# Optimization experiments

Hardware: AMD Instinct MI355X
Metric: run time of the kernel (lower is better)

The kernel has to match this reference:

```python
import jax, jax.numpy as jnp
import numpy as np

DELTA_A, DELTA_R = 0.1, 1.0
ALPHA, BETA, GAMMA = 1.0, 1.0, 0.001


def setup_inputs() -> dict:
    key = jax.random.key(0)
    B, D, H, W, K = 4, 32, 512, 512, 16
    out = jax.random.normal(key, (B, D, H, W), dtype=jnp.float32)
    # 4x4 block partition -> K=16 instance labels, one center per block
    gh, gw = 4, 4
    bh, bw = H // gh, W // gw
    rows = np.arange(H) // bh  # [H]
    cols = np.arange(W) // bw  # [W]
    labels = (rows[:, None] * gw + cols[None, :]).astype(np.int32)  # [H,W]
    target = jnp.asarray(np.broadcast_to(labels, (B, H, W)).copy())
    ctr = np.array([[r * bh + bh // 2, c * bw + bw // 2]
                    for r in range(gh) for c in range(gw)], dtype=np.int32)  # [K,2]
    centers = jnp.asarray(np.broadcast_to(ctr, (B, K, 2)).copy())
    return {"out": out, "target": target, "centers": centers, "batch_size": B}


def _safe_sqrt(x):
    # matches torch.linalg.norm subgradient 0 at 0 (avoids NaN grads)
    pos = x > 0
    return jnp.where(pos, jnp.sqrt(jnp.where(pos, x, 1.0)), 0.0)


def _pairwise_norm(a, b):
    # a [M,D], b [N,D] -> [M,N] euclidean distances via gram trick
    d2 = (jnp.sum(a * a, 1)[:, None] + jnp.sum(b * b, 1)[None, :]
          - 2.0 * a @ b.T)
    return _safe_sqrt(jax.nn.relu(d2))


def _per_image(o, t, c):
    # o [D,H,W], t [H,W] int, c [K,2] int
    D = o.shape[0]
    K = c.shape[0]
    x = o.reshape(D, -1).T                      # [HW, D]
    E = o[:, c[:, 0], c[:, 1]].T                # [K, D] center embeddings
    lab_c = t[c[:, 0], c[:, 1]]                 # [K]
    mask = (t.reshape(-1)[None, :] == lab_c[:, None])  # [K, HW]
    # attraction: hinged distance of every cluster pixel to its center
    norms = _pairwise_norm(E, x)                # [K, HW]
    hinged = jax.nn.relu(norms - DELTA_A) * mask
    cnt = jnp.sum(mask, axis=1)
    denom = jnp.maximum(cnt - 1, 1).astype(o.dtype)
    s_att = jnp.sum(jnp.sum(hinged, axis=1) / denom)
    # repelling: pairwise center distances; diagonal contributes relu(delta_r)
    # per row and the original subtracts delta_r per center -> excluded
    nE = _pairwise_norm(E, E)                   # [K, K]
    s_rep = jnp.sum(jax.nn.relu(DELTA_R - nE)) - K * DELTA_R
    # regularization: norm of each center embedding
    s_reg = jnp.sum(_safe_sqrt(jnp.sum(E * E, axis=1)))
    return s_att, s_rep, s_reg


def reference(out, target, centers, batch_size):
    K = centers.shape[1]
    s_att, s_rep, s_reg = jax.vmap(_per_image)(out, target, centers)  # [B] each
    div_att = jnp.float32(K)
    div_rep = jnp.float32(K * (K - 1))
    div_reg = jnp.float32(K)

    def step(carry, s):
        a, r, g = carry
        sa, sr, sg = s
        return ((a + sa) / div_att, (r + sr) / div_rep, (g + sg) / div_reg), None

    zero = jnp.float32(0.0)
    (att, rep, reg), _ = jax.lax.scan(step, (zero, zero, zero),
                                      (s_att, s_rep, s_reg))
    loss = ALPHA * att + BETA * rep + GAMMA * reg
    return loss, att, rep
```

## Files before the change

kernel.cpp:

```cpp
#include <hip/hip_runtime.h>
#include <hip/hip_bf16.h>

#define B_ 4
#define D_ 32
#define H_ 512
#define W_ 512
#define K_ 16
#define N_ (H_ * W_)
#define NQ_ (N_ / 4)
#define NBLK_ 256
#define EPAD 33

#define WS_SUM  0
#define WS_CNT  64
#define WS_E2   128
#define WS_LAB  192
#define WS_E    264
#define WS_PART 4096

typedef float vfloat4 __attribute__((ext_vector_type(4)));
typedef int vint4 __attribute__((ext_vector_type(4)));

__device__ inline vfloat4 nt_load_f4(const float* p) {
  return __builtin_nontemporal_load((const vfloat4*)p);
}
__device__ inline vint4 nt_load_i4(const int* p) {
  return __builtin_nontemporal_load((const vint4*)p);
}

__global__ __launch_bounds__(64) void setup_kernel(
    const float* __restrict__ outp, const int* __restrict__ target,
    const int* __restrict__ centers, float* __restrict__ ws) {
  const int b = blockIdx.x, k = blockIdx.y;
  const int lane = threadIdx.x;
  const int cy = centers[(b * K_ + k) * 2 + 0];
  const int cx = centers[(b * K_ + k) * 2 + 1];
  float v = 0.0f;
  if (lane < D_) {
    v = outp[(((size_t)b * D_ + lane) * H_ + cy) * W_ + cx];
    ws[WS_E + (b * K_ + k) * D_ + lane] = v;
  }
  float s = v * v;
  for (int off = 32; off > 0; off >>= 1) s += __shfl_xor(s, off, 64);
  if (lane == 0) {
    ws[WS_E2 + b * K_ + k] = s;
    ((int*)ws)[WS_LAB + b * K_ + k] = target[(size_t)b * N_ + cy * W_ + cx];
  }
}

__global__ __launch_bounds__(256) void attract_kernel(
    const float* __restrict__ outp, const int* __restrict__ target,
    float* __restrict__ ws) {
  const int b = blockIdx.y;
  const int tid = threadIdx.x;
  __shared__ float sE[K_ * EPAD];
  __shared__ float se2[K_];
  __shared__ int slab[K_];
  __shared__ float bs[K_];
  __shared__ float bc[K_];

  if (tid < 128) {
    const vfloat4 v = *(const vfloat4*)(ws + WS_E + b * (K_ * D_) + tid * 4);
    const int k = tid >> 3, d = (tid & 7) * 4;
    sE[k * EPAD + d + 0] = v.x;
    sE[k * EPAD + d + 1] = v.y;
    sE[k * EPAD + d + 2] = v.z;
    sE[k * EPAD + d + 3] = v.w;
  }
  if (tid < K_) {
    se2[tid] = ws[WS_E2 + b * K_ + tid];
    slab[tid] = ((const int*)ws)[WS_LAB + b * K_ + tid];
    bs[tid] = 0.0f;
    bc[tid] = 0.0f;
  }
  __syncthreads();

  const int q = blockIdx.x * 256 + tid;
  const float* xb = outp + (size_t)b * D_ * N_;
  const vint4 lab4 = nt_load_i4(target + (size_t)b * N_ + 4 * q);
  const int labv[4] = {lab4.x, lab4.y, lab4.z, lab4.w};

  int kf[4], nm[4];
#pragma unroll
  for (int j = 0; j < 4; ++j) { kf[j] = 0; nm[j] = 0; }
#pragma unroll
  for (int k = 0; k < K_; ++k) {
    const int lk = slab[k];
#pragma unroll
    for (int j = 0; j < 4; ++j) {
      if (labv[j] == lk) { if (nm[j] == 0) kf[j] = k; nm[j]++; }
    }
  }

  float dot[4] = {0.f, 0.f, 0.f, 0.f};
  float x2[4] = {0.f, 0.f, 0.f, 0.f};
#pragma unroll
  for (int d = 0; d < D_; ++d) {
    const vfloat4 x = nt_load_f4(xb + (size_t)d * N_ + 4 * q);
    const float xs[4] = {x.x, x.y, x.z, x.w};
#pragma unroll
    for (int j = 0; j < 4; ++j) {
      const float e = sE[kf[j] * EPAD + d];
      dot[j] = fmaf(xs[j], e, dot[j]);
      x2[j] = fmaf(xs[j], xs[j], x2[j]);
    }
  }

  float hv[4];
#pragma unroll
  for (int j = 0; j < 4; ++j) {
    const float d2 = x2[j] + se2[kf[j]] - 2.0f * dot[j];
    const float h = fmaxf(sqrtf(fmaxf(d2, 0.0f)) - 0.1f, 0.0f);
    hv[j] = (nm[j] > 0) ? h : 0.0f;
  }
  const bool same = (kf[0] == kf[1]) & (kf[1] == kf[2]) & (kf[2] == kf[3]);
  if (same) {
    const float cs = (float)((nm[0] > 0) + (nm[1] > 0) + (nm[2] > 0) + (nm[3] > 0));
    if (cs > 0.0f) {
      atomicAdd(&bs[kf[0]], hv[0] + hv[1] + hv[2] + hv[3]);
      atomicAdd(&bc[kf[0]], cs);
    }
  } else {
#pragma unroll
    for (int j = 0; j < 4; ++j) {
      if (nm[j] > 0) {
        atomicAdd(&bs[kf[j]], hv[j]);
        atomicAdd(&bc[kf[j]], 1.0f);
      }
    }
  }

  const bool extra = (nm[0] > 1) | (nm[1] > 1) | (nm[2] > 1) | (nm[3] > 1);
  if (__any(extra)) {
    for (int k = 0; k < K_; ++k) {
      bool need[4]; bool anyn = false;
#pragma unroll
      for (int j = 0; j < 4; ++j) {
        need[j] = (nm[j] > 1) && (labv[j] == slab[k]) && (k != kf[j]);
        anyn |= need[j];
      }
      if (__any(anyn)) {
        float dt[4] = {0.f, 0.f, 0.f, 0.f};
        for (int d = 0; d < D_; ++d) {
          const vfloat4 x = nt_load_f4(xb + (size_t)d * N_ + 4 * q);
          const float e = sE[k * EPAD + d];
          dt[0] = fmaf(x.x, e, dt[0]);
          dt[1] = fmaf(x.y, e, dt[1]);
          dt[2] = fmaf(x.z, e, dt[2]);
          dt[3] = fmaf(x.w, e, dt[3]);
        }
#pragma unroll
        for (int j = 0; j < 4; ++j) {
          if (need[j]) {
            const float d2 = x2[j] + se2[k] - 2.0f * dt[j];
            atomicAdd(&bs[k], fmaxf(sqrtf(fmaxf(d2, 0.0f)) - 0.1f, 0.0f));
            atomicAdd(&bc[k], 1.0f);
          }
        }
      }
    }
  }
  __syncthreads();

  if (tid < 2 * K_) {
    float* p = ws + WS_PART + ((size_t)b * NBLK_ + blockIdx.x) * (2 * K_);
    p[tid] = (tid < K_) ? bs[tid] : bc[tid - K_];
  }
}

__global__ __launch_bounds__(256) void reduce_kernel(const float* __restrict__ ws_in,
                                                     float* __restrict__ ws) {
  const int b = blockIdx.x >> 4, k = blockIdx.x & 15;
  const int tid = threadIdx.x;
  const float* base = ws_in + WS_PART + (size_t)b * NBLK_ * (2 * K_);
  float s = 0.0f, c = 0.0f;
  for (int i = tid; i < NBLK_; i += 256) {
    s += base[i * (2 * K_) + k];
    c += base[i * (2 * K_) + K_ + k];
  }
  for (int off = 32; off > 0; off >>= 1) {
    s += __shfl_xor(s, off, 64);
    c += __shfl_xor(c, off, 64);
  }
  __shared__ float rs[4], rc[4];
  if ((tid & 63) == 0) { rs[tid >> 6] = s; rc[tid >> 6] = c; }
  __syncthreads();
  if (tid == 0) {
    ws[WS_SUM + b * K_ + k] = rs[0] + rs[1] + rs[2] + rs[3];
    ws[WS_CNT + b * K_ + k] = rc[0] + rc[1] + rc[2] + rc[3];
  }
}

__global__ __launch_bounds__(256) void final_kernel(const float* __restrict__ ws,
                                                    float* __restrict__ out) {
  __shared__ float sE[B_ * K_ * D_];
  __shared__ float sred[256];
  __shared__ float srep[B_];
  __shared__ float sreg[B_];
  __shared__ float ssa[B_];
  const int tid = threadIdx.x;
  for (int i = tid; i < B_ * K_ * D_; i += 256) sE[i] = ws[WS_E + i];
  __syncthreads();

  const int i = tid >> 4, j = tid & 15;
  for (int b = 0; b < B_; ++b) {
    float dotv = 0.0f;
#pragma unroll 8
    for (int d = 0; d < D_; ++d)
      dotv = fmaf(sE[(b * K_ + i) * D_ + d], sE[(b * K_ + j) * D_ + d], dotv);
    const float d2 = ws[WS_E2 + b * K_ + i] + ws[WS_E2 + b * K_ + j] - 2.0f * dotv;
    sred[tid] = fmaxf(1.0f - sqrtf(fmaxf(d2, 0.0f)), 0.0f);
    __syncthreads();
    for (int s = 128; s > 0; s >>= 1) {
      if (tid < s) sred[tid] += sred[tid + s];
      __syncthreads();
    }
    if (tid == 0) srep[b] = sred[0] - (float)K_;
    __syncthreads();
  }

  sred[tid] = (tid < B_ * K_) ? sqrtf(fmaxf(ws[WS_E2 + tid], 0.0f)) : 0.0f;
  __syncthreads();
  if (tid < B_) {
    float s = 0.0f;
    for (int k = 0; k < K_; ++k) s += sred[tid * K_ + k];
    sreg[tid] = s;
  }

  if (tid < B_ * K_) {
    const float c = ws[WS_CNT + tid];
    float v = ws[WS_SUM + tid] / fmaxf(c - 1.0f, 1.0f);
    for (int off = 1; off < K_; off <<= 1) v += __shfl_xor(v, off, 64);
    if ((tid & 15) == 0) ssa[tid >> 4] = v;
  }
  __syncthreads();

  if (tid == 0) {
    float att = 0.0f, rep = 0.0f, reg = 0.0f;
    for (int b = 0; b < B_; ++b) {
      att = (att + ssa[b]) / (float)K_;
      rep = (rep + srep[b]) / (float)(K_ * (K_ - 1));
      reg = (reg + sreg[b]) / (float)K_;
    }
    out[0] = att + rep + 0.001f * reg;
    out[1] = att;
    out[2] = rep;
  }
}

extern "C" void kernel_launch(void* const* d_in, const int* in_sizes, int n_in,
                              void* d_out, int out_size, void* d_ws, size_t ws_size,
                              hipStream_t stream) {
  const float* outp = (const float*)d_in[0];
  const int* target = (const int*)d_in[1];
  const int* centers = (const int*)d_in[2];
  float* ws = (float*)d_ws;
  float* out = (float*)d_out;

  setup_kernel<<<dim3(B_, K_), 64, 0, stream>>>(outp, target, centers, ws);
  attract_kernel<<<dim3(NBLK_, B_), 256, 0, stream>>>(outp, target, ws);
  reduce_kernel<<<dim3(B_ * K_), 256, 0, stream>>>(ws, ws);
  final_kernel<<<1, 256, 0, stream>>>(ws, out);
}
```

Baseline: 200.2 us.

## Add wave-uniform fast path and fold partial reduction into final kernel

Adds a fast path in the attraction kernel for waves whose half-waves each cover a single cluster. In that path the center embedding is read from a uniform global pointer instead of per-lane LDS lookups, and the hinged sums are reduced with shuffles before a single atomic per half-wave. The separate reduce kernel is removed and its per-block partial reduction moved into the single-block final kernel, saving a launch at the cost of a serial reduction in one block. Also sets launch-bounds occupancy hints.

```diff
diff --git a/kernel.cpp b/kernel.cpp
--- a/kernel.cpp
+++ b/kernel.cpp
@@ -48,7 +48,7 @@
   }
 }
 
-__global__ __launch_bounds__(256) void attract_kernel(
+__global__ __launch_bounds__(256, 4) void attract_kernel(
     const float* __restrict__ outp, const int* __restrict__ target,
     float* __restrict__ ws) {
   const int b = blockIdx.y;
@@ -92,69 +92,94 @@
     }
   }
 
-  float dot[4] = {0.f, 0.f, 0.f, 0.f};
-  float x2[4] = {0.f, 0.f, 0.f, 0.f};
-#pragma unroll
-  for (int d = 0; d < D_; ++d) {
-    const vfloat4 x = nt_load_f4(xb + (size_t)d * N_ + 4 * q);
-    const float xs[4] = {x.x, x.y, x.z, x.w};
+  const int lane = tid & 63;
+  const bool thread_ok =
+      (nm[0] == 1) & (nm[1] == 1) & (nm[2] == 1) & (nm[3] == 1) &
+      (kf[1] == kf[0]) & (kf[2] == kf[0]) & (kf[3] == kf[0]);
+  const int kA = __builtin_amdgcn_readfirstlane(kf[0]);
+  const int kB = __shfl(kf[0], 32, 64);
+  const bool low = lane < 32;
+  const bool half_ok = kf[0] == (low ? kA : kB);
+  const bool fast = __all(thread_ok & half_ok);
+
+  if (fast) {
+    const float* __restrict__ eA = ws + WS_E + (b * K_ + kA) * D_;
+    const float* __restrict__ eB = ws + WS_E + (b * K_ + __builtin_amdgcn_readfirstlane(kB)) * D_;
+    float dot[4] = {0.f, 0.f, 0.f, 0.f};
+    float x2[4] = {0.f, 0.f, 0.f, 0.f};
+#pragma unroll 8
+    for (int d = 0; d < D_; ++d) {
+      const vfloat4 x = nt_load_f4(xb + (size_t)d * N_ + 4 * q);
+      const float e = low ? eA[d] : eB[d];
+      dot[0] = fmaf(x.x, e, dot[0]);
+      x2[0] = fmaf(x.x, x.x, x2[0]);
+      dot[1] = fmaf(x.y, e, dot[1]);
+      x2[1] = fmaf(x.y, x.y, x2[1]);
+      dot[2] = fmaf(x.z, e, dot[2]);
+      x2[2] = fmaf(x.z, x.z, x2[2]);
+      dot[3] = fmaf(x.w, e, dot[3]);
+      x2[3] = fmaf(x.w, x.w, x2[3]);
+    }
+    const float e2k = se2[kf[0]];
+    float hq = 0.0f;
 #pragma unroll
     for (int j = 0; j < 4; ++j) {
-      const float e = sE[kf[j] * EPAD + d];
-      dot[j] = fmaf(xs[j], e, dot[j]);
-      x2[j] = fmaf(xs[j], xs[j], x2[j]);
-    }
-  }
-
-  float hv[4];
-#pragma unroll
-  for (int j = 0; j < 4; ++j) {
-    const float d2 = x2[j] + se2[kf[j]] - 2.0f * dot[j];
-    const float h = fmaxf(sqrtf(fmaxf(d2, 0.0f)) - 0.1f, 0.0f);
-    hv[j] = (nm[j] > 0) ? h : 0.0f;
-  }
-  const bool same = (kf[0] == kf[1]) & (kf[1] == kf[2]) & (kf[2] == kf[3]);
-  if (same) {
-    const float cs = (float)((nm[0] > 0) + (nm[1] > 0) + (nm[2] > 0) + (nm[3] > 0));
-    if (cs > 0.0f) {
-      atomicAdd(&bs[kf[0]], hv[0] + hv[1] + hv[2] + hv[3]);
-      atomicAdd(&bc[kf[0]], cs);
+      const float d2 = x2[j] + e2k - 2.0f * dot[j];
+      hq += fmaxf(sqrtf(fmaxf(d2, 0.0f)) - 0.1f, 0.0f);
+    }
+    for (int off = 16; off > 0; off >>= 1) hq += __shfl_xor(hq, off, 64);
+    if ((lane & 31) == 0) {
+      atomicAdd(&bs[kf[0]], hq);
+      atomicAdd(&bc[kf[0]], 128.0f);
     }
   } else {
+    float dot[4] = {0.f, 0.f, 0.f, 0.f};
+    float x2[4] = {0.f, 0.f, 0.f, 0.f};
+#pragma unroll 8
+    for (int d = 0; d < D_; ++d) {
+      const vfloat4 x = nt_load_f4(xb + (size_t)d * N_ + 4 * q);
+      const float xs[4] = {x.x, x.y, x.z, x.w};
+#pragma unroll
+      for (int j = 0; j < 4; ++j) {
+        const float e = sE[kf[j] * EPAD + d];
+        dot[j] = fmaf(xs[j], e, dot[j]);
+        x2[j] = fmaf(xs[j], xs[j], x2[j]);
+      }
+    }
 #pragma unroll
     for (int j = 0; j < 4; ++j) {
       if (nm[j] > 0) {
-        atomicAdd(&bs[kf[j]], hv[j]);
+        const float d2 = x2[j] + se2[kf[j]] - 2.0f * dot[j];
+        atomicAdd(&bs[kf[j]], fmaxf(sqrtf(fmaxf(d2, 0.0f)) - 0.1f, 0.0f));
         atomicAdd(&bc[kf[j]], 1.0f);
       }
     }
-  }
-
-  const bool extra = (nm[0] > 1) | (nm[1] > 1) | (nm[2] > 1) | (nm[3] > 1);
-  if (__any(extra)) {
-    for (int k = 0; k < K_; ++k) {
-      bool need[4]; bool anyn = false;
-#pragma unroll
-      for (int j = 0; j < 4; ++j) {
-        need[j] = (nm[j] > 1) && (labv[j] == slab[k]) && (k != kf[j]);
-        anyn |= need[j];
-      }
-      if (__any(anyn)) {
-        float dt[4] = {0.f, 0.f, 0.f, 0.f};
-        for (int d = 0; d < D_; ++d) {
-          const vfloat4 x = nt_load_f4(xb + (size_t)d * N_ + 4 * q);
-          const float e = sE[k * EPAD + d];
-          dt[0] = fmaf(x.x, e, dt[0]);
-          dt[1] = fmaf(x.y, e, dt[1]);
-          dt[2] = fmaf(x.z, e, dt[2]);
-          dt[3] = fmaf(x.w, e, dt[3]);
+    const bool extra = (nm[0] > 1) | (nm[1] > 1) | (nm[2] > 1) | (nm[3] > 1);
+    if (__any(extra)) {
+      for (int k = 0; k < K_; ++k) {
+        bool need[4]; bool anyn = false;
+#pragma unroll
+        for (int j = 0; j < 4; ++j) {
+          need[j] = (nm[j] > 1) && (labv[j] == slab[k]) && (k != kf[j]);
+          anyn |= need[j];
         }
-#pragma unroll
-        for (int j = 0; j < 4; ++j) {
-          if (need[j]) {
-            const float d2 = x2[j] + se2[k] - 2.0f * dt[j];
-            atomicAdd(&bs[k], fmaxf(sqrtf(fmaxf(d2, 0.0f)) - 0.1f, 0.0f));
-            atomicAdd(&bc[k], 1.0f);
+        if (__any(anyn)) {
+          float dt[4] = {0.f, 0.f, 0.f, 0.f};
+          for (int d = 0; d < D_; ++d) {
+            const vfloat4 x = nt_load_f4(xb + (size_t)d * N_ + 4 * q);
+            const float e = sE[k * EPAD + d];
+            dt[0] = fmaf(x.x, e, dt[0]);
+            dt[1] = fmaf(x.y, e, dt[1]);
+            dt[2] = fmaf(x.z, e, dt[2]);
+            dt[3] = fmaf(x.w, e, dt[3]);
+          }
+#pragma unroll
+          for (int j = 0; j < 4; ++j) {
+            if (need[j]) {
+              const float d2 = x2[j] + se2[k] - 2.0f * dt[j];
+              atomicAdd(&bs[k], fmaxf(sqrtf(fmaxf(d2, 0.0f)) - 0.1f, 0.0f));
+              atomicAdd(&bc[k], 1.0f);
+            }
           }
         }
       }
@@ -165,29 +190,6 @@
   if (tid < 2 * K_) {
     float* p = ws + WS_PART + ((size_t)b * NBLK_ + blockIdx.x) * (2 * K_);
     p[tid] = (tid < K_) ? bs[tid] : bc[tid - K_];
-  }
-}
-
-__global__ __launch_bounds__(256) void reduce_kernel(const float* __restrict__ ws_in,
-                                                     float* __restrict__ ws) {
-  const int b = blockIdx.x >> 4, k = blockIdx.x & 15;
-  const int tid = threadIdx.x;
-  const float* base = ws_in + WS_PART + (size_t)b * NBLK_ * (2 * K_);
-  float s = 0.0f, c = 0.0f;
-  for (int i = tid; i < NBLK_; i += 256) {
-    s += base[i * (2 * K_) + k];
-    c += base[i * (2 * K_) + K_ + k];
-  }
-  for (int off = 32; off > 0; off >>= 1) {
-    s += __shfl_xor(s, off, 64);
-    c += __shfl_xor(c, off, 64);
-  }
-  __shared__ float rs[4], rc[4];
-  if ((tid & 63) == 0) { rs[tid >> 6] = s; rc[tid >> 6] = c; }
-  __syncthreads();
-  if (tid == 0) {
-    ws[WS_SUM + b * K_ + k] = rs[0] + rs[1] + rs[2] + rs[3];
-    ws[WS_CNT + b * K_ + k] = rc[0] + rc[1] + rc[2] + rc[3];
   }
 }
 
@@ -195,11 +197,32 @@
                                                     float* __restrict__ out) {
   __shared__ float sE[B_ * K_ * D_];
   __shared__ float sred[256];
+  __shared__ float scred[256];
+  __shared__ float ssum[B_ * K_];
+  __shared__ float scnt[B_ * K_];
   __shared__ float srep[B_];
   __shared__ float sreg[B_];
   __shared__ float ssa[B_];
   const int tid = threadIdx.x;
+
+  {
+    const int p = tid >> 2, sub = tid & 3;
+    const int bb = p >> 4, kk = p & 15;
+    const float* base = ws + WS_PART + (size_t)bb * NBLK_ * (2 * K_);
+    float s = 0.0f, c = 0.0f;
+    for (int i = sub; i < NBLK_; i += 4) {
+      s += base[i * (2 * K_) + kk];
+      c += base[i * (2 * K_) + K_ + kk];
+    }
+    sred[tid] = s;
+    scred[tid] = c;
+  }
   for (int i = tid; i < B_ * K_ * D_; i += 256) sE[i] = ws[WS_E + i];
+  __syncthreads();
+  if (tid < B_ * K_) {
+    ssum[tid] = sred[tid * 4] + sred[tid * 4 + 1] + sred[tid * 4 + 2] + sred[tid * 4 + 3];
+    scnt[tid] = scred[tid * 4] + scred[tid * 4 + 1] + scred[tid * 4 + 2] + scred[tid * 4 + 3];
+  }
   __syncthreads();
 
   const int i = tid >> 4, j = tid & 15;
@@ -228,8 +251,7 @@
   }
 
   if (tid < B_ * K_) {
-    const float c = ws[WS_CNT + tid];
-    float v = ws[WS_SUM + tid] / fmaxf(c - 1.0f, 1.0f);
+    float v = ssum[tid] / fmaxf(scnt[tid] - 1.0f, 1.0f);
     for (int off = 1; off < K_; off <<= 1) v += __shfl_xor(v, off, 64);
     if ((tid & 15) == 0) ssa[tid >> 4] = v;
   }
@@ -259,6 +281,5 @@
 
   setup_kernel<<<dim3(B_, K_), 64, 0, stream>>>(outp, target, centers, ws);
   attract_kernel<<<dim3(NBLK_, B_), 256, 0, stream>>>(outp, target, ws);
-  reduce_kernel<<<dim3(B_ * K_), 256, 0, stream>>>(ws, ws);
   final_kernel<<<1, 256, 0, stream>>>(ws, out);
 }
```

Result: slower. 220.2 us (+10.0%).

## Fold setup and reduce kernels into attract and final kernels

Applied to the files above, without the earlier changes.

Removes the separate setup and reduce launches. Each attract block now gathers its own center embeddings, labels and squared norms from the input. The final kernel regathers the centers and reduces the per-block partials itself. This cuts two kernel launches and their inter-kernel dependencies, at the cost of redundant center gathers in every attract block and a heavier single-block final kernel. The main D loop unroll is also capped at 16.

```diff
diff --git a/kernel.cpp b/kernel.cpp
--- a/kernel.cpp
+++ b/kernel.cpp
@@ -11,12 +11,7 @@
 #define NBLK_ 256
 #define EPAD 33
 
-#define WS_SUM  0
-#define WS_CNT  64
-#define WS_E2   128
-#define WS_LAB  192
-#define WS_E    264
-#define WS_PART 4096
+#define WS_PART 0
 
 typedef float vfloat4 __attribute__((ext_vector_type(4)));
 typedef int vint4 __attribute__((ext_vector_type(4)));
@@ -28,29 +23,9 @@
   return __builtin_nontemporal_load((const vint4*)p);
 }
 
-__global__ __launch_bounds__(64) void setup_kernel(
+__global__ __launch_bounds__(256) void attract_kernel(
     const float* __restrict__ outp, const int* __restrict__ target,
     const int* __restrict__ centers, float* __restrict__ ws) {
-  const int b = blockIdx.x, k = blockIdx.y;
-  const int lane = threadIdx.x;
-  const int cy = centers[(b * K_ + k) * 2 + 0];
-  const int cx = centers[(b * K_ + k) * 2 + 1];
-  float v = 0.0f;
-  if (lane < D_) {
-    v = outp[(((size_t)b * D_ + lane) * H_ + cy) * W_ + cx];
-    ws[WS_E + (b * K_ + k) * D_ + lane] = v;
-  }
-  float s = v * v;
-  for (int off = 32; off > 0; off >>= 1) s += __shfl_xor(s, off, 64);
-  if (lane == 0) {
-    ws[WS_E2 + b * K_ + k] = s;
-    ((int*)ws)[WS_LAB + b * K_ + k] = target[(size_t)b * N_ + cy * W_ + cx];
-  }
-}
-
-__global__ __launch_bounds__(256) void attract_kernel(
-    const float* __restrict__ outp, const int* __restrict__ target,
-    float* __restrict__ ws) {
   const int b = blockIdx.y;
   const int tid = threadIdx.x;
   __shared__ float sE[K_ * EPAD];
@@ -59,19 +34,25 @@
   __shared__ float bs[K_];
   __shared__ float bc[K_];
 
-  if (tid < 128) {
-    const vfloat4 v = *(const vfloat4*)(ws + WS_E + b * (K_ * D_) + tid * 4);
-    const int k = tid >> 3, d = (tid & 7) * 4;
-    sE[k * EPAD + d + 0] = v.x;
-    sE[k * EPAD + d + 1] = v.y;
-    sE[k * EPAD + d + 2] = v.z;
-    sE[k * EPAD + d + 3] = v.w;
+  for (int i = tid; i < K_ * D_; i += 256) {
+    const int k = i >> 5, d = i & 31;
+    const int cy = centers[(b * K_ + k) * 2 + 0];
+    const int cx = centers[(b * K_ + k) * 2 + 1];
+    sE[k * EPAD + d] = outp[(((size_t)b * D_ + d) * H_ + cy) * W_ + cx];
   }
   if (tid < K_) {
-    se2[tid] = ws[WS_E2 + b * K_ + tid];
-    slab[tid] = ((const int*)ws)[WS_LAB + b * K_ + tid];
+    const int cy = centers[(b * K_ + tid) * 2 + 0];
+    const int cx = centers[(b * K_ + tid) * 2 + 1];
+    slab[tid] = target[(size_t)b * N_ + cy * W_ + cx];
     bs[tid] = 0.0f;
     bc[tid] = 0.0f;
+  }
+  __syncthreads();
+  if (tid < K_) {
+    float s = 0.0f;
+#pragma unroll
+    for (int d = 0; d < D_; ++d) s = fmaf(sE[tid * EPAD + d], sE[tid * EPAD + d], s);
+    se2[tid] = s;
   }
   __syncthreads();
 
@@ -94,7 +75,7 @@
 
   float dot[4] = {0.f, 0.f, 0.f, 0.f};
   float x2[4] = {0.f, 0.f, 0.f, 0.f};
-#pragma unroll
+#pragma unroll 16
   for (int d = 0; d < D_; ++d) {
     const vfloat4 x = nt_load_f4(xb + (size_t)d * N_ + 4 * q);
     const float xs[4] = {x.x, x.y, x.z, x.w};
@@ -168,38 +149,49 @@
   }
 }
 
-__global__ __launch_bounds__(256) void reduce_kernel(const float* __restrict__ ws_in,
-                                                     float* __restrict__ ws) {
-  const int b = blockIdx.x >> 4, k = blockIdx.x & 15;
-  const int tid = threadIdx.x;
-  const float* base = ws_in + WS_PART + (size_t)b * NBLK_ * (2 * K_);
-  float s = 0.0f, c = 0.0f;
-  for (int i = tid; i < NBLK_; i += 256) {
-    s += base[i * (2 * K_) + k];
-    c += base[i * (2 * K_) + K_ + k];
-  }
-  for (int off = 32; off > 0; off >>= 1) {
-    s += __shfl_xor(s, off, 64);
-    c += __shfl_xor(c, off, 64);
-  }
-  __shared__ float rs[4], rc[4];
-  if ((tid & 63) == 0) { rs[tid >> 6] = s; rc[tid >> 6] = c; }
-  __syncthreads();
-  if (tid == 0) {
-    ws[WS_SUM + b * K_ + k] = rs[0] + rs[1] + rs[2] + rs[3];
-    ws[WS_CNT + b * K_ + k] = rc[0] + rc[1] + rc[2] + rc[3];
-  }
-}
-
-__global__ __launch_bounds__(256) void final_kernel(const float* __restrict__ ws,
-                                                    float* __restrict__ out) {
+__global__ __launch_bounds__(256) void final_kernel(
+    const float* __restrict__ outp, const int* __restrict__ centers,
+    const float* __restrict__ ws, float* __restrict__ out) {
   __shared__ float sE[B_ * K_ * D_];
+  __shared__ float se2[B_ * K_];
   __shared__ float sred[256];
+  __shared__ float scred[256];
+  __shared__ float ssum[B_ * K_];
+  __shared__ float scnt[B_ * K_];
   __shared__ float srep[B_];
   __shared__ float sreg[B_];
   __shared__ float ssa[B_];
   const int tid = threadIdx.x;
-  for (int i = tid; i < B_ * K_ * D_; i += 256) sE[i] = ws[WS_E + i];
+
+  for (int i = tid; i < B_ * K_ * D_; i += 256) {
+    const int bk = i >> 5, d = i & 31;
+    const int b = bk >> 4, k = bk & 15;
+    const int cy = centers[(b * K_ + k) * 2 + 0];
+    const int cx = centers[(b * K_ + k) * 2 + 1];
+    sE[i] = outp[(((size_t)b * D_ + d) * H_ + cy) * W_ + cx];
+  }
+
+  {
+    const int p = tid >> 2, sub = tid & 3;
+    const int bb = p >> 4, kk = p & 15;
+    const float* base = ws + WS_PART + (size_t)bb * NBLK_ * (2 * K_);
+    float s = 0.0f, c = 0.0f;
+    for (int i = sub; i < NBLK_; i += 4) {
+      s += base[i * (2 * K_) + kk];
+      c += base[i * (2 * K_) + K_ + kk];
+    }
+    sred[tid] = s;
+    scred[tid] = c;
+  }
+  __syncthreads();
+  if (tid < B_ * K_) {
+    ssum[tid] = sred[tid * 4] + sred[tid * 4 + 1] + sred[tid * 4 + 2] + sred[tid * 4 + 3];
+    scnt[tid] = scred[tid * 4] + scred[tid * 4 + 1] + scred[tid * 4 + 2] + scred[tid * 4 + 3];
+    float s = 0.0f;
+#pragma unroll
+    for (int d = 0; d < D_; ++d) s = fmaf(sE[tid * D_ + d], sE[tid * D_ + d], s);
+    se2[tid] = s;
+  }
   __syncthreads();
 
   const int i = tid >> 4, j = tid & 15;
@@ -208,7 +200,7 @@
 #pragma unroll 8
     for (int d = 0; d < D_; ++d)
       dotv = fmaf(sE[(b * K_ + i) * D_ + d], sE[(b * K_ + j) * D_ + d], dotv);
-    const float d2 = ws[WS_E2 + b * K_ + i] + ws[WS_E2 + b * K_ + j] - 2.0f * dotv;
+    const float d2 = se2[b * K_ + i] + se2[b * K_ + j] - 2.0f * dotv;
     sred[tid] = fmaxf(1.0f - sqrtf(fmaxf(d2, 0.0f)), 0.0f);
     __syncthreads();
     for (int s = 128; s > 0; s >>= 1) {
@@ -219,7 +211,7 @@
     __syncthreads();
   }
 
-  sred[tid] = (tid < B_ * K_) ? sqrtf(fmaxf(ws[WS_E2 + tid], 0.0f)) : 0.0f;
+  sred[tid] = (tid < B_ * K_) ? sqrtf(fmaxf(se2[tid], 0.0f)) : 0.0f;
   __syncthreads();
   if (tid < B_) {
     float s = 0.0f;
@@ -228,8 +220,7 @@
   }
 
   if (tid < B_ * K_) {
-    const float c = ws[WS_CNT + tid];
-    float v = ws[WS_SUM + tid] / fmaxf(c - 1.0f, 1.0f);
+    float v = ssum[tid] / fmaxf(scnt[tid] - 1.0f, 1.0f);
     for (int off = 1; off < K_; off <<= 1) v += __shfl_xor(v, off, 64);
     if ((tid & 15) == 0) ssa[tid >> 4] = v;
   }
@@ -257,8 +248,6 @@
   float* ws = (float*)d_ws;
   float* out = (float*)d_out;
 
-  setup_kernel<<<dim3(B_, K_), 64, 0, stream>>>(outp, target, centers, ws);
-  attract_kernel<<<dim3(NBLK_, B_), 256, 0, stream>>>(outp, target, ws);
-  reduce_kernel<<<dim3(B_ * K_), 256, 0, stream>>>(ws, ws);
-  final_kernel<<<1, 256, 0, stream>>>(ws, out);
-}
+  attract_kernel<<<dim3(NBLK_, B_), 256, 0, stream>>>(outp, target, centers, ws);
+  final_kernel<<<1, 256, 0, stream>>>(outp, centers, ws, out);
+}
```

After: 216.1 us. +8.0%, slower.
